# Optimization experiments

Measured on AMD Instinct MI355X. Metric: run time of the kernel, lower is better.

The kernel has to match this reference:

```python
import jax, jax.numpy as jnp
import numpy as np

# dims
B, Nt, Ln, Lv = 16, 64, 256, 4      # batch, trees/batch, nodes/tree, value tokens/node
D = 256                              # embedding_dim
VOCAB, NTYPE = 32000, 64
M, Ls = 128, 4                       # story memory slots, tokens per slot
HOPS = 3                             # max_hops
COMP_STEP = 4                        # max tree depth = max(kb_n_layers)
LEVELS = [0, 1, 16, 64, 160, Ln]     # node index ranges per depth 0..4


def setup_inputs() -> dict:
    rng = np.random.default_rng(0)
    key = jax.random.key(0)
    ks = jax.random.split(key, 12)

    # --- tree structure: depth per node, father index in previous level ---
    depth = np.zeros(Ln, np.int64)
    father = np.zeros((B, Nt, Ln), np.int64)
    for lvl in range(1, 5):
        lo, hi = LEVELS[lvl], LEVELS[lvl + 1]
        depth[lo:hi] = lvl
        father[..., lo:hi] = rng.integers(LEVELS[lvl - 1], LEVELS[lvl], (B, Nt, hi - lo))
    father[..., 0] = Ln  # root's father = pad slot (torch -1 wraps to last index)
    kb_fathers = np.concatenate([father, np.full((B, Nt, 1), Ln, np.int64)], -1)  # [B,Nt,Ln+1]
    nl = np.broadcast_to(depth, (B, Nt, Ln))
    kb_n_layers = np.concatenate([nl, np.full((B, Nt, 1), -1, np.int64)], -1)     # [B,Nt,Ln+1]

    kb_values = rng.integers(1, VOCAB, (B, Nt, Ln, Lv))
    kb_types = rng.integers(1, NTYPE, (B, Nt, Ln))
    story = rng.integers(1, VOCAB, (B, M, Ls))
    decoder_input = rng.integers(1, VOCAB, (B,))

    s = 1.0 / np.sqrt(D)
    C = 0.1 * jax.random.normal(ks[0], (HOPS + 1, VOCAB, D), jnp.float32)
    C = C.at[:, 0].set(0.0)  # padding_idx = 0
    T_emb = 0.1 * jax.random.normal(ks[1], (NTYPE, D), jnp.float32)
    T_emb = T_emb.at[0].set(0.0)
    return {
        'decoder_input': jnp.asarray(decoder_input),
        'story': jnp.asarray(story),
        'hidden': 0.1 * jax.random.normal(ks[2], (1, B, D), jnp.float32),
        'kb_values': jnp.asarray(kb_values),
        'kb_types': jnp.asarray(kb_types),
        'kb_fathers': jnp.asarray(kb_fathers),
        'kb_n_layers': jnp.asarray(kb_n_layers),
        'C': C,
        'T_emb': T_emb,
        'Wq': s * jax.random.normal(ks[3], (D, D), jnp.float32),
        'Wk': s * jax.random.normal(ks[4], (D, D), jnp.float32),
        'Wv': s * jax.random.normal(ks[5], (D, D), jnp.float32),
        'W1_w': s * jax.random.normal(ks[6], (VOCAB, 2 * D), jnp.float32),
        'W1_b': jnp.zeros((VOCAB,), jnp.float32),
        'W_ih': s * jax.random.normal(ks[7], (3 * D, D), jnp.float32),
        'W_hh': s * jax.random.normal(ks[8], (3 * D, D), jnp.float32),
        'b_ih': jnp.zeros((3 * D,), jnp.float32),
        'b_hh': jnp.zeros((3 * D,), jnp.float32),
    }


def _forward(decoder_input, story, hidden, kb_values, kb_types, kb_fathers, kb_n_layers,
             C, T_emb, Wq, Wk, Wv, W1_w, W1_b, W_ih, W_hh, b_ih, b_hh):
    C0 = C[0]
    # ensemble: node embed = type_embed * sum(value token embeds)   [B,Nt,Ln,D]
    node = T_emb[kb_types] * C0[kb_values].sum(-2)
    node = jnp.concatenate([node, jnp.zeros((B, Nt, 1, D), node.dtype)], axis=2)  # pad slot
    nl = COMP_STEP - 1 - kb_n_layers  # adjusted layer counter
    base = jnp.arange(B * Nt).reshape(B, Nt, 1) * (Ln + 1)
    seg = (base + kb_fathers).reshape(-1)  # flat father ids for scatter-add

    def body(i, carry):
        node, nl = carry
        nxt = jax.ops.segment_sum(node.reshape(-1, D), seg,
                                  num_segments=B * Nt * (Ln + 1)).reshape(B, Nt, Ln + 1, D)
        node = node + nxt * (nl == 0)[..., None].astype(node.dtype)
        return (node, nl - 1)

    node, _ = jax.lax.fori_loop(0, COMP_STEP, body, (node, nl))
    roots = node[:, :, 0]                                   # [B,Nt,D]
    bias = jnp.where(roots.sum(-1) == 0, -1e9, 0.0)         # attention_bias [B,Nt]

    # compute_global_ranking: QKV attention over tree roots
    h = hidden[-1]                                          # [B,D]
    w = jax.nn.softmax(jnp.einsum('bnd,bd->bn', roots @ Wk.T, h @ Wq.T) + bias, axis=1)
    feat = jnp.einsum('bn,bnd->bd', w, roots @ Wv.T)        # kb_attn_features

    # single GRU step (PyTorch gate order r,z,n)
    x = C0[decoder_input]
    gi = x @ W_ih.T + b_ih
    gh = h @ W_hh.T + b_hh
    ir, iz, inn = jnp.split(gi, 3, -1)
    hr, hz, hn = jnp.split(gh, 3, -1)
    r = jax.nn.sigmoid(ir + hr)
    z = jax.nn.sigmoid(iz + hz)
    n = jnp.tanh(inn + r * hn)
    h_new = (1.0 - z) * n + z * h
    u = h_new + feat                                        # cur_state

    # ptrMemDecoder (Mem2Seq-style hops over story memory)
    p_vocab = None
    logits = None
    for hop in range(HOPS):
        m_A = C[hop][story].sum(2)                          # [B,M,D]
        logits = jnp.einsum('bmd,bd->bm', m_A, u)
        prob = jax.nn.softmax(logits, axis=1)
        m_C = C[hop + 1][story].sum(2)
        o = jnp.einsum('bm,bmd->bd', prob, m_C)
        if hop == 0:
            p_vocab = jnp.concatenate([u, o], -1) @ W1_w.T + W1_b
        u = u + o
    p_ptr = logits
    return p_ptr, p_vocab, h_new


def reference(decoder_input, story, hidden, kb_values, kb_types, kb_fathers, kb_n_layers,
              C, T_emb, Wq, Wk, Wv, W1_w, W1_b, W_ih, W_hh, b_ih, b_hh):
    return _forward(decoder_input, story, hidden, kb_values, kb_types, kb_fathers, kb_n_layers,
                    C, T_emb, Wq, Wk, Wv, W1_w, W1_b, W_ih, W_hh, b_ih, b_hh)
```

## Files before the change

### kernel.cpp

```cpp
#include <hip/hip_runtime.h>
#include <hip/hip_bf16.h>
#include <math.h>

#define B_ 16
#define NT 64
#define LN 256
#define LV 4
#define D_ 256
#define VOCAB_ 32000
#define M_ 128
#define LS 4

typedef unsigned short ushort_t;
typedef unsigned int uint_t;

__device__ __forceinline__ ushort_t f2bf(float f) {
  uint_t u = __float_as_uint(f);
  uint_t r = u + 0x7FFFu + ((u >> 16) & 1u);
  return (ushort_t)(r >> 16);
}
__device__ __forceinline__ float bflo(uint_t u) {
  return __uint_as_float(u << 16);
}
__device__ __forceinline__ float bfhi(uint_t u) {
  return __uint_as_float(u & 0xFFFF0000u);
}

#define NB_S (3 * B_ * M_)
#define NB_CONV 2048
#define NB_TR 192
#define NB_TQK 256
#define NB_WVT 64
__global__ __launch_bounds__(256) void k_prep(
    const int* __restrict__ story, const float* __restrict__ C,
    const float* __restrict__ W_ih, const float* __restrict__ W_hh,
    const float* __restrict__ Wq, const float* __restrict__ Wk,
    const float* __restrict__ Wv, float* __restrict__ S,
    ushort_t* __restrict__ C0h, float* __restrict__ W_ihT,
    float* __restrict__ W_hhT, float* __restrict__ TQK,
    float* __restrict__ WvT) {
  __shared__ float smem[32 * 33];
  int blk = blockIdx.x, tid = threadIdx.x;
  if (blk < NB_S) {
    int h = blk / (B_ * M_);
    int bm = blk % (B_ * M_);
    const int* st = story + (size_t)bm * LS;
    const float* Ch = C + (size_t)h * VOCAB_ * D_;
    float s = Ch[(size_t)st[0] * D_ + tid] + Ch[(size_t)st[1] * D_ + tid] +
              Ch[(size_t)st[2] * D_ + tid] + Ch[(size_t)st[3] * D_ + tid];
    S[(size_t)blk * D_ + tid] = s;
  } else if (blk < NB_S + NB_CONV) {
    int n4 = VOCAB_ * D_ / 4;
    for (int i = (blk - NB_S) * 256 + tid; i < n4; i += NB_CONV * 256) {
      float4 f = ((const float4*)C)[i];
      uint2 packed;
      packed.x = (uint_t)f2bf(f.x) | ((uint_t)f2bf(f.y) << 16);
      packed.y = (uint_t)f2bf(f.z) | ((uint_t)f2bf(f.w) << 16);
      ((uint2*)C0h)[i] = packed;
    }
  } else if (blk < NB_S + NB_CONV + 2 * NB_TR) {
    int t = blk - (NB_S + NB_CONV);
    const float* W = W_ih;
    float* WT = W_ihT;
    if (t >= NB_TR) { t -= NB_TR; W = W_hh; WT = W_hhT; }
    const int R = 768;
    int tr = t % (R / 32), tc = t / (R / 32);
    int tx = tid & 31, ty = tid >> 5;
#pragma unroll
    for (int k = 0; k < 4; ++k)
      smem[(ty + 8 * k) * 33 + tx] =
          W[(size_t)(tr * 32 + ty + 8 * k) * D_ + tc * 32 + tx];
    __syncthreads();
#pragma unroll
    for (int k = 0; k < 4; ++k)
      WT[(size_t)(tc * 32 + ty + 8 * k) * R + tr * 32 + tx] =
          smem[tx * 33 + ty + 8 * k];
  } else if (blk < NB_S + NB_CONV + 2 * NB_TR + NB_TQK) {
    int j = blk - (NB_S + NB_CONV + 2 * NB_TR);
    smem[tid] = Wq[(size_t)tid * D_ + j];
    __syncthreads();
    float acc = 0.f;
#pragma unroll 8
    for (int k = 0; k < D_; ++k) acc += smem[k] * Wk[(size_t)k * D_ + tid];
    TQK[(size_t)j * D_ + tid] = acc;
  } else {
    int t = blk - (NB_S + NB_CONV + 2 * NB_TR + NB_TQK);
    int tr = t & 7, tc = t >> 3;
    int tx = tid & 31, ty = tid >> 5;
#pragma unroll
    for (int k = 0; k < 4; ++k)
      smem[(ty + 8 * k) * 33 + tx] =
          Wv[(size_t)(tr * 32 + ty + 8 * k) * D_ + tc * 32 + tx];
    __syncthreads();
#pragma unroll
    for (int k = 0; k < 4; ++k)
      WvT[(size_t)(tc * 32 + ty + 8 * k) * D_ + tr * 32 + tx] =
          smem[tx * 33 + ty + 8 * k];
  }
}

__global__ __launch_bounds__(256) void k_rootsg(
    const int* __restrict__ kb_values, const int* __restrict__ kb_types,
    const ushort_t* __restrict__ C0h, const float* __restrict__ T_emb,
    const int* __restrict__ dec, const float* __restrict__ C0,
    const float* __restrict__ hidden, const float* __restrict__ W_ihT,
    const float* __restrict__ W_hhT, const float* __restrict__ TQK,
    const float* __restrict__ b_ih, const float* __restrict__ b_hh,
    float* __restrict__ part, float* __restrict__ gi, float* __restrict__ gh,
    float* __restrict__ tvec) {
  __shared__ __align__(16) char smem_raw[16384];
  int blk = blockIdx.x, tid = threadIdx.x;
  if (blk < 2048) {
    int bn = blk >> 1;
    int half = blk & 1;
    int lane = tid & 63, team = tid >> 6;
    int* sv = (int*)smem_raw;
    int* st = (int*)(smem_raw + 2048);
    float* psum = (float*)(smem_raw + 2560);
    const int* vptr = kb_values + (size_t)bn * LN * LV + half * 128 * LV;
    for (int i = tid; i < 128 * LV; i += 256) sv[i] = vptr[i];
    if (tid < 128) st[tid] = kb_types[(size_t)bn * LN + half * 128 + tid];
    __syncthreads();
    float a0 = 0.f, a1 = 0.f, a2 = 0.f, a3 = 0.f;
#pragma unroll 4
    for (int li = 0; li < 32; ++li) {
      int l = team * 32 + li;
      int4 v = ((const int4*)sv)[l];
      uint2 u0 = ((const uint2*)(C0h + (size_t)v.x * D_))[lane];
      uint2 u1 = ((const uint2*)(C0h + (size_t)v.y * D_))[lane];
      uint2 u2 = ((const uint2*)(C0h + (size_t)v.z * D_))[lane];
      uint2 u3 = ((const uint2*)(C0h + (size_t)v.w * D_))[lane];
      float4 t4 = ((const float4*)(T_emb + (size_t)st[l] * D_))[lane];
      float s0 = bflo(u0.x) + bflo(u1.x) + bflo(u2.x) + bflo(u3.x);
      float s1 = bfhi(u0.x) + bfhi(u1.x) + bfhi(u2.x) + bfhi(u3.x);
      float s2 = bflo(u0.y) + bflo(u1.y) + bflo(u2.y) + bflo(u3.y);
      float s3 = bfhi(u0.y) + bfhi(u1.y) + bfhi(u2.y) + bfhi(u3.y);
      a0 += t4.x * s0;
      a1 += t4.y * s1;
      a2 += t4.z * s2;
      a3 += t4.w * s3;
    }
    psum[team * D_ + 4 * lane + 0] = a0;
    psum[team * D_ + 4 * lane + 1] = a1;
    psum[team * D_ + 4 * lane + 2] = a2;
    psum[team * D_ + 4 * lane + 3] = a3;
    __syncthreads();
    float r = psum[0 * D_ + tid] + psum[1 * D_ + tid] + psum[2 * D_ + tid] +
              psum[3 * D_ + tid];
    part[((size_t)bn * 2 + half) * D_ + tid] = r;
  } else {
    int g = blk - 2048;
    float* xs = (float*)smem_raw;
    float acc[B_];
    if (g < 3) {
#pragma unroll
      for (int b = 0; b < B_; ++b)
        xs[b * D_ + tid] = C0[(size_t)dec[b] * D_ + tid];
      __syncthreads();
      int i = g * 256 + tid;
      float bias = b_ih[i];
#pragma unroll
      for (int b = 0; b < B_; ++b) acc[b] = bias;
#pragma unroll 4
      for (int j = 0; j < D_; ++j) {
        float w = W_ihT[(size_t)j * 768 + i];
#pragma unroll
        for (int b = 0; b < B_; ++b) acc[b] += xs[b * D_ + j] * w;
      }
#pragma unroll
      for (int b = 0; b < B_; ++b) gi[(size_t)b * 768 + i] = acc[b];
    } else if (g < 6) {
#pragma unroll
      for (int b = 0; b < B_; ++b) xs[b * D_ + tid] = hidden[b * D_ + tid];
      __syncthreads();
      int i = (g - 3) * 256 + tid;
      float bias = b_hh[i];
#pragma unroll
      for (int b = 0; b < B_; ++b) acc[b] = bias;
#pragma unroll 4
      for (int j = 0; j < D_; ++j) {
        float w = W_hhT[(size_t)j * 768 + i];
#pragma unroll
        for (int b = 0; b < B_; ++b) acc[b] += xs[b * D_ + j] * w;
      }
#pragma unroll
      for (int b = 0; b < B_; ++b) gh[(size_t)b * 768 + i] = acc[b];
    } else {
#pragma unroll
      for (int b = 0; b < B_; ++b) xs[b * D_ + tid] = hidden[b * D_ + tid];
      __syncthreads();
#pragma unroll
      for (int b = 0; b < B_; ++b) acc[b] = 0.f;
#pragma unroll 4
      for (int j = 0; j < D_; ++j) {
        float w = TQK[(size_t)j * D_ + tid];
#pragma unroll
        for (int b = 0; b < B_; ++b) acc[b] += xs[b * D_ + j] * w;
      }
#pragma unroll
      for (int b = 0; b < B_; ++b) tvec[b * D_ + tid] = acc[b];
    }
  }
}

__global__ __launch_bounds__(256) void k_mid(
    const float* __restrict__ part, const float* __restrict__ tvec,
    const float* __restrict__ S, float* __restrict__ scores,
    float* __restrict__ ST) {
  int blk = blockIdx.x, tid = threadIdx.x;
  if (blk < 1024) {
    int b = blk >> 6;
    const float* p = part + (size_t)blk * 2 * D_;
    float rv = p[tid] + p[D_ + tid];
    float sc = rv * tvec[b * D_ + tid];
    float sm = rv;
    __shared__ float red[8];
    int lane = tid & 63, wave = tid >> 6;
    for (int o = 32; o > 0; o >>= 1) {
      sc += __shfl_xor(sc, o);
      sm += __shfl_xor(sm, o);
    }
    if (lane == 0) { red[wave] = sc; red[4 + wave] = sm; }
    __syncthreads();
    if (tid == 0) {
      float SC = red[0] + red[1] + red[2] + red[3];
      float SM = red[4] + red[5] + red[6] + red[7];
      scores[blk] = (SM == 0.0f) ? SC - 1000000000.0f : SC;
    }
  } else {
    int t = blk - 1024;
    int hb = t >> 5;
    int tile = t & 31;
    int tm = tile & 3, td = tile >> 2;
    int tx = tid & 31, ty = tid >> 5;
    __shared__ float sm2[32 * 33];
    const float* Sp = S + (size_t)hb * M_ * D_;
    float* STp = ST + (size_t)hb * D_ * M_;
#pragma unroll
    for (int k = 0; k < 4; ++k)
      sm2[(ty + 8 * k) * 33 + tx] =
          Sp[(size_t)(tm * 32 + ty + 8 * k) * D_ + td * 32 + tx];
    __syncthreads();
#pragma unroll
    for (int k = 0; k < 4; ++k)
      STp[(size_t)(td * 32 + ty + 8 * k) * M_ + tm * 32 + tx] =
          sm2[tx * 33 + ty + 8 * k];
  }
}

__global__ __launch_bounds__(256) void k_chain(
    const float* __restrict__ scores, const float* __restrict__ part,
    const float* __restrict__ WvT, const float* __restrict__ gi,
    const float* __restrict__ gh, const float* __restrict__ hidden,
    const float* __restrict__ S, const float* __restrict__ ST,
    float* __restrict__ h_new_out, float* __restrict__ cat,
    float* __restrict__ p_ptr) {
  int b = blockIdx.x, tid = threadIdx.x;
  __shared__ float wsh[NT], rs[D_], us[D_], lo[M_], loB[M_], pr[M_];
  if (tid < NT) {
    float s = scores[b * NT + tid];
    float m = s;
    for (int o = 32; o > 0; o >>= 1) m = fmaxf(m, __shfl_xor(m, o));
    float e = expf(s - m);
    float sum = e;
    for (int o = 32; o > 0; o >>= 1) sum += __shfl_xor(sum, o);
    wsh[tid] = e / sum;
  }
  __syncthreads();
  float rb = 0.f;
#pragma unroll 16
  for (int n = 0; n < NT; ++n) {
    const float* p = part + ((size_t)(b * NT + n) * 2) * D_;
    rb += wsh[n] * (p[tid] + p[D_ + tid]);
  }
  rs[tid] = rb;
  __syncthreads();
  float feat = 0.f;
#pragma unroll 16
  for (int j = 0; j < D_; ++j) feat += rs[j] * WvT[(size_t)j * D_ + tid];
  {
    float i_r = gi[(size_t)b * 768 + tid];
    float i_z = gi[(size_t)b * 768 + 256 + tid];
    float i_n = gi[(size_t)b * 768 + 512 + tid];
    float h_r = gh[(size_t)b * 768 + tid];
    float h_z = gh[(size_t)b * 768 + 256 + tid];
    float h_n = gh[(size_t)b * 768 + 512 + tid];
    float h = hidden[b * D_ + tid];
    float r = 1.f / (1.f + expf(-(i_r + h_r)));
    float z = 1.f / (1.f + expf(-(i_z + h_z)));
    float nn = tanhf(i_n + r * h_n);
    float hn = (1.f - z) * nn + z * h;
    h_new_out[b * D_ + tid] = hn;
    float u0 = hn + feat;
    us[tid] = u0;
    cat[b * 512 + tid] = u0;
  }
  __syncthreads();
  for (int h = 0; h < 3; ++h) {
    {
      int m = tid & 127;
      int half = tid >> 7;
      const float* STp = ST + (((size_t)h * B_ + b) * D_ + half * 128) * M_;
      float l = 0.f;
#pragma unroll 16
      for (int d = 0; d < 128; ++d)
        l += us[half * 128 + d] * STp[(size_t)d * M_ + m];
      if (half == 0) lo[m] = l; else loB[m] = l;
    }
    __syncthreads();
    if (h == 2) {
      if (tid < M_) p_ptr[b * M_ + tid] = lo[tid] + loB[tid];
      break;
    }
    if (tid < 64) {
      float l0 = lo[tid] + loB[tid], l1 = lo[tid + 64] + loB[tid + 64];
      float a = fmaxf(l0, l1);
      for (int o = 32; o > 0; o >>= 1) a = fmaxf(a, __shfl_xor(a, o));
      float e0 = expf(l0 - a), e1 = expf(l1 - a);
      float s = e0 + e1;
      for (int o = 32; o > 0; o >>= 1) s += __shfl_xor(s, o);
      pr[tid] = e0 / s;
      pr[tid + 64] = e1 / s;
    }
    __syncthreads();
    {
      const float* Sn = S + (((size_t)(h + 1) * B_ + b) * M_) * D_;
      float o = 0.f;
#pragma unroll 16
      for (int m = 0; m < M_; ++m) o += pr[m] * Sn[(size_t)m * D_ + tid];
      if (h == 0) cat[b * 512 + D_ + tid] = o;
      us[tid] += o;
    }
    __syncthreads();
  }
}

__global__ __launch_bounds__(256) void k_pvocab(
    const float* __restrict__ cat, const float* __restrict__ W1_w,
    const float* __restrict__ W1_b, float* __restrict__ out) {
  int blk = blockIdx.x, tid = threadIdx.x;
  int row = tid & 63, q = tid >> 6;
  int v = blk * 64 + row;
  __shared__ float cs[B_ * 512];
  __shared__ float ps[3][64][B_];
  for (int i = tid; i < B_ * 512; i += 256) cs[i] = cat[i];
  __syncthreads();
  const float4* wrow = (const float4*)(W1_w + (size_t)v * 512 + q * 128);
  float acc[B_];
#pragma unroll
  for (int b = 0; b < B_; ++b) acc[b] = 0.f;
#pragma unroll 4
  for (int k4 = 0; k4 < 32; ++k4) {
    float4 w = wrow[k4];
#pragma unroll
    for (int b = 0; b < B_; ++b) {
      const float* c = &cs[b * 512 + q * 128 + k4 * 4];
      acc[b] += w.x * c[0] + w.y * c[1] + w.z * c[2] + w.w * c[3];
    }
  }
  if (q > 0) {
#pragma unroll
    for (int b = 0; b < B_; ++b) ps[q - 1][row][b] = acc[b];
  }
  __syncthreads();
  if (q == 0) {
    float bb = W1_b[v];
#pragma unroll
    for (int b = 0; b < B_; ++b)
      out[(size_t)b * VOCAB_ + v] =
          acc[b] + ps[0][row][b] + ps[1][row][b] + ps[2][row][b] + bb;
  }
}

extern "C" void kernel_launch(void* const* d_in, const int* in_sizes, int n_in,
                              void* d_out, int out_size, void* d_ws,
                              size_t ws_size, hipStream_t stream) {
  const int* decoder_input = (const int*)d_in[0];
  const int* story = (const int*)d_in[1];
  const float* hidden = (const float*)d_in[2];
  const int* kb_values = (const int*)d_in[3];
  const int* kb_types = (const int*)d_in[4];
  const float* C = (const float*)d_in[7];
  const float* T_emb = (const float*)d_in[8];
  const float* Wq = (const float*)d_in[9];
  const float* Wk = (const float*)d_in[10];
  const float* Wv = (const float*)d_in[11];
  const float* W1_w = (const float*)d_in[12];
  const float* W1_b = (const float*)d_in[13];
  const float* W_ih = (const float*)d_in[14];
  const float* W_hh = (const float*)d_in[15];
  const float* b_ih = (const float*)d_in[16];
  const float* b_hh = (const float*)d_in[17];

  float* out = (float*)d_out;
  float* p_ptr = out;
  float* p_vocab = out + B_ * M_;
  float* h_new = out + B_ * M_ + B_ * VOCAB_;

  float* ws = (float*)d_ws;
  float* S = ws;
  float* part = S + 3 * B_ * M_ * D_;
  float* cat = part + B_ * NT * 2 * D_;
  float* scores = cat + B_ * 512;
  float* gi = scores + B_ * NT;
  float* gh = gi + B_ * 768;
  float* tvec = gh + B_ * 768;
  ushort_t* C0h = (ushort_t*)(tvec + B_ * D_);
  float* wtmp = (float*)(C0h + (size_t)VOCAB_ * D_);
  float* W_ihT = wtmp;
  float* W_hhT = W_ihT + 768 * D_;
  float* TQK = W_hhT + 768 * D_;
  float* ST = wtmp;
  float* WvT = wtmp + 3 * B_ * M_ * D_;

  hipLaunchKernelGGL(k_prep,
                     dim3(NB_S + NB_CONV + 2 * NB_TR + NB_TQK + NB_WVT),
                     dim3(256), 0, stream, story, C, W_ih, W_hh, Wq, Wk, Wv, S,
                     C0h, W_ihT, W_hhT, TQK, WvT);
  hipLaunchKernelGGL(k_rootsg, dim3(2048 + 7), dim3(256), 0, stream, kb_values,
                     kb_types, C0h, T_emb, decoder_input, C, hidden, W_ihT,
                     W_hhT, TQK, b_ih, b_hh, part, gi, gh, tvec);
  hipLaunchKernelGGL(k_mid, dim3(1024 + 1536), dim3(256), 0, stream, part,
                     tvec, S, scores, ST);
  hipLaunchKernelGGL(k_chain, dim3(B_), dim3(256), 0, stream, scores, part,
                     WvT, gi, gh, hidden, S, ST, h_new, cat, p_ptr);
  hipLaunchKernelGGL(k_pvocab, dim3(VOCAB_ / 64), dim3(256), 0, stream, cat,
                     W1_w, W1_b, p_vocab);
}
```

Baseline: 389.2 us.

## Partition bf16 embedding table by column slice and assign root blocks per XCC

The bf16 copy of the embedding table is stored as eight 32-column slices, so each slice (about 2 MB) can stay resident in one XCC's L2. The root-feature kernel now runs 8×1024 blocks. Each block reads its hardware XCC id and claims a (slice, tree) work item through per-slice atomic counters, preferring the slice owned by its own XCC. It then computes 32 columns of the type-weighted value-sum for that tree with the type embeddings staged in shared memory. The goal is to turn random gathers over the whole table into L2-local accesses, at the cost of atomics, a memset and many more small blocks.

```diff
diff --git a/kernel.cpp b/kernel.cpp
--- a/kernel.cpp
+++ b/kernel.cpp
@@ -53,10 +53,14 @@
     int n4 = VOCAB_ * D_ / 4;
     for (int i = (blk - NB_S) * 256 + tid; i < n4; i += NB_CONV * 256) {
       float4 f = ((const float4*)C)[i];
+      int v = i >> 6;
+      int c4 = i & 63;
+      int g = c4 >> 3;
+      int o = c4 & 7;
       uint2 packed;
       packed.x = (uint_t)f2bf(f.x) | ((uint_t)f2bf(f.y) << 16);
       packed.y = (uint_t)f2bf(f.z) | ((uint_t)f2bf(f.w) << 16);
-      ((uint2*)C0h)[i] = packed;
+      ((uint2*)C0h)[(size_t)g * VOCAB_ * 8 + (size_t)v * 8 + o] = packed;
     }
   } else if (blk < NB_S + NB_CONV + 2 * NB_TR) {
     int t = blk - (NB_S + NB_CONV);
@@ -99,57 +103,73 @@
   }
 }
 
-__global__ __launch_bounds__(256) void k_rootsg(
+__global__ __launch_bounds__(256) void k_rootsx(
     const int* __restrict__ kb_values, const int* __restrict__ kb_types,
     const ushort_t* __restrict__ C0h, const float* __restrict__ T_emb,
-    const int* __restrict__ dec, const float* __restrict__ C0,
-    const float* __restrict__ hidden, const float* __restrict__ W_ihT,
-    const float* __restrict__ W_hhT, const float* __restrict__ TQK,
-    const float* __restrict__ b_ih, const float* __restrict__ b_hh,
-    float* __restrict__ part, float* __restrict__ gi, float* __restrict__ gh,
-    float* __restrict__ tvec) {
-  __shared__ __align__(16) char smem_raw[16384];
+    int* __restrict__ cnt, const int* __restrict__ dec,
+    const float* __restrict__ C0, const float* __restrict__ hidden,
+    const float* __restrict__ W_ihT, const float* __restrict__ W_hhT,
+    const float* __restrict__ TQK, const float* __restrict__ b_ih,
+    const float* __restrict__ b_hh, float* __restrict__ roots,
+    float* __restrict__ gi, float* __restrict__ gh, float* __restrict__ tvec) {
+  __shared__ __align__(16) char smem_raw[18944];
+  __shared__ int claim;
   int blk = blockIdx.x, tid = threadIdx.x;
-  if (blk < 2048) {
-    int bn = blk >> 1;
-    int half = blk & 1;
-    int lane = tid & 63, team = tid >> 6;
+  if (blk >= 7) {
+    if (tid == 0) {
+      int xcc = __builtin_amdgcn_s_getreg((31 << 11) | 20) & 7;
+      int got = -1;
+      for (int a = 0; a < 8; ++a) {
+        int g = (xcc + a) & 7;
+        int bn = atomicAdd(&cnt[g], 1);
+        if (bn < 1024) { got = (g << 10) | bn; break; }
+      }
+      claim = got;
+    }
+    __syncthreads();
+    int cl = claim;
+    if (cl < 0) return;
+    int g = cl >> 10, bn = cl & 1023;
     int* sv = (int*)smem_raw;
-    int* st = (int*)(smem_raw + 2048);
-    float* psum = (float*)(smem_raw + 2560);
-    const int* vptr = kb_values + (size_t)bn * LN * LV + half * 128 * LV;
-    for (int i = tid; i < 128 * LV; i += 256) sv[i] = vptr[i];
-    if (tid < 128) st[tid] = kb_types[(size_t)bn * LN + half * 128 + tid];
-    __syncthreads();
+    int* st = (int*)(smem_raw + 4096);
+    float* ts = (float*)(smem_raw + 5120);
+    float* psum = (float*)(smem_raw + 14336);
+    const int* vptr = kb_values + (size_t)bn * LN * LV;
+    for (int i = tid; i < LN * LV; i += 256) sv[i] = vptr[i];
+    st[tid] = kb_types[(size_t)bn * LN + tid];
+    for (int idx = tid; idx < 64 * 32; idx += 256) {
+      int t = idx >> 5, c = idx & 31;
+      ts[t * 36 + c] = T_emb[t * D_ + g * 32 + c];
+    }
+    __syncthreads();
+    int r = tid >> 3, cp = tid & 7;
+    const ushort_t* slice = C0h + (size_t)g * VOCAB_ * 32;
     float a0 = 0.f, a1 = 0.f, a2 = 0.f, a3 = 0.f;
 #pragma unroll 4
-    for (int li = 0; li < 32; ++li) {
-      int l = team * 32 + li;
-      int4 v = ((const int4*)sv)[l];
-      uint2 u0 = ((const uint2*)(C0h + (size_t)v.x * D_))[lane];
-      uint2 u1 = ((const uint2*)(C0h + (size_t)v.y * D_))[lane];
-      uint2 u2 = ((const uint2*)(C0h + (size_t)v.z * D_))[lane];
-      uint2 u3 = ((const uint2*)(C0h + (size_t)v.w * D_))[lane];
-      float4 t4 = ((const float4*)(T_emb + (size_t)st[l] * D_))[lane];
-      float s0 = bflo(u0.x) + bflo(u1.x) + bflo(u2.x) + bflo(u3.x);
-      float s1 = bfhi(u0.x) + bfhi(u1.x) + bfhi(u2.x) + bfhi(u3.x);
-      float s2 = bflo(u0.y) + bflo(u1.y) + bflo(u2.y) + bflo(u3.y);
-      float s3 = bfhi(u0.y) + bfhi(u1.y) + bfhi(u2.y) + bfhi(u3.y);
-      a0 += t4.x * s0;
-      a1 += t4.y * s1;
-      a2 += t4.z * s2;
-      a3 += t4.w * s3;
-    }
-    psum[team * D_ + 4 * lane + 0] = a0;
-    psum[team * D_ + 4 * lane + 1] = a1;
-    psum[team * D_ + 4 * lane + 2] = a2;
-    psum[team * D_ + 4 * lane + 3] = a3;
-    __syncthreads();
-    float r = psum[0 * D_ + tid] + psum[1 * D_ + tid] + psum[2 * D_ + tid] +
-              psum[3 * D_ + tid];
-    part[((size_t)bn * 2 + half) * D_ + tid] = r;
+    for (int i = 0; i < 32; ++i) {
+      int vIdx = i * 32 + r;
+      int v = sv[vIdx];
+      int t = st[vIdx >> 2];
+      uint2 u = *(const uint2*)(slice + (size_t)v * 32 + cp * 4);
+      const float* tw = &ts[t * 36 + cp * 4];
+      a0 += tw[0] * bflo(u.x);
+      a1 += tw[1] * bfhi(u.x);
+      a2 += tw[2] * bflo(u.y);
+      a3 += tw[3] * bfhi(u.y);
+    }
+    psum[r * 36 + cp * 4 + 0] = a0;
+    psum[r * 36 + cp * 4 + 1] = a1;
+    psum[r * 36 + cp * 4 + 2] = a2;
+    psum[r * 36 + cp * 4 + 3] = a3;
+    __syncthreads();
+    if (tid < 32) {
+      float s = 0.f;
+#pragma unroll
+      for (int rr = 0; rr < 32; ++rr) s += psum[rr * 36 + tid];
+      roots[(size_t)bn * D_ + g * 32 + tid] = s;
+    }
   } else {
-    int g = blk - 2048;
+    int g = blk;
     float* xs = (float*)smem_raw;
     float acc[B_];
     if (g < 3) {
@@ -204,14 +224,13 @@
 }
 
 __global__ __launch_bounds__(256) void k_mid(
-    const float* __restrict__ part, const float* __restrict__ tvec,
+    const float* __restrict__ roots, const float* __restrict__ tvec,
     const float* __restrict__ S, float* __restrict__ scores,
     float* __restrict__ ST) {
   int blk = blockIdx.x, tid = threadIdx.x;
   if (blk < 1024) {
     int b = blk >> 6;
-    const float* p = part + (size_t)blk * 2 * D_;
-    float rv = p[tid] + p[D_ + tid];
+    float rv = roots[(size_t)blk * D_ + tid];
     float sc = rv * tvec[b * D_ + tid];
     float sm = rv;
     __shared__ float red[8];
@@ -249,7 +268,7 @@
 }
 
 __global__ __launch_bounds__(256) void k_chain(
-    const float* __restrict__ scores, const float* __restrict__ part,
+    const float* __restrict__ scores, const float* __restrict__ roots,
     const float* __restrict__ WvT, const float* __restrict__ gi,
     const float* __restrict__ gh, const float* __restrict__ hidden,
     const float* __restrict__ S, const float* __restrict__ ST,
@@ -269,10 +288,8 @@
   __syncthreads();
   float rb = 0.f;
 #pragma unroll 16
-  for (int n = 0; n < NT; ++n) {
-    const float* p = part + ((size_t)(b * NT + n) * 2) * D_;
-    rb += wsh[n] * (p[tid] + p[D_ + tid]);
-  }
+  for (int n = 0; n < NT; ++n)
+    rb += wsh[n] * roots[((size_t)(b * NT + n)) * D_ + tid];
   rs[tid] = rb;
   __syncthreads();
   float feat = 0.f;
@@ -399,13 +416,14 @@
 
   float* ws = (float*)d_ws;
   float* S = ws;
-  float* part = S + 3 * B_ * M_ * D_;
-  float* cat = part + B_ * NT * 2 * D_;
+  float* roots = S + 3 * B_ * M_ * D_;
+  float* cat = roots + B_ * NT * D_;
   float* scores = cat + B_ * 512;
   float* gi = scores + B_ * NT;
   float* gh = gi + B_ * 768;
   float* tvec = gh + B_ * 768;
-  ushort_t* C0h = (ushort_t*)(tvec + B_ * D_);
+  int* cnt = (int*)(tvec + B_ * D_);
+  ushort_t* C0h = (ushort_t*)(cnt + 16);
   float* wtmp = (float*)(C0h + (size_t)VOCAB_ * D_);
   float* W_ihT = wtmp;
   float* W_hhT = W_ihT + 768 * D_;
@@ -413,16 +431,18 @@
   float* ST = wtmp;
   float* WvT = wtmp + 3 * B_ * M_ * D_;
 
+  hipMemsetAsync(cnt, 0, 16 * sizeof(int), stream);
   hipLaunchKernelGGL(k_prep,
                      dim3(NB_S + NB_CONV + 2 * NB_TR + NB_TQK + NB_WVT),
                      dim3(256), 0, stream, story, C, W_ih, W_hh, Wq, Wk, Wv, S,
                      C0h, W_ihT, W_hhT, TQK, WvT);
-  hipLaunchKernelGGL(k_rootsg, dim3(2048 + 7), dim3(256), 0, stream, kb_values,
-                     kb_types, C0h, T_emb, decoder_input, C, hidden, W_ihT,
-                     W_hhT, TQK, b_ih, b_hh, part, gi, gh, tvec);
-  hipLaunchKernelGGL(k_mid, dim3(1024 + 1536), dim3(256), 0, stream, part,
+  hipLaunchKernelGGL(k_rootsx, dim3(7 + 8 * 1024), dim3(256), 0, stream,
+                     kb_values, kb_types, C0h, T_emb, cnt, decoder_input, C,
+                     hidden, W_ihT, W_hhT, TQK, b_ih, b_hh, roots, gi, gh,
+                     tvec);
+  hipLaunchKernelGGL(k_mid, dim3(1024 + 1536), dim3(256), 0, stream, roots,
                      tvec, S, scores, ST);
-  hipLaunchKernelGGL(k_chain, dim3(B_), dim3(256), 0, stream, scores, part,
+  hipLaunchKernelGGL(k_chain, dim3(B_), dim3(256), 0, stream, scores, roots,
                      WvT, gi, gh, hidden, S, ST, h_new, cat, p_ptr);
   hipLaunchKernelGGL(k_pvocab, dim3(VOCAB_ / 64), dim3(256), 0, stream, cat,
                      W1_w, W1_b, p_vocab);
```

Measured after the change: 417.6 us. 1.07x slower.
